# Kernel tuning notes

Hardware: AMD Instinct MI355X
Metric: run time of the kernel (lower is better)

Reference implementation:

```python
import jax, jax.numpy as jnp
import numpy as np

NUM_HEADS = 8
NEG_INF = -1e9  # stand-in for -inf in the causal mask (avoids nan under masked softmax)


def setup_inputs() -> dict:
    key = jax.random.key(0)
    ks = jax.random.split(key, 8)
    B, C, H, W = 2, 512, 64, 64
    E = 512
    s = 1.0 / np.sqrt(C)
    return {
        "query": jax.random.normal(ks[0], (B, C, H, W), jnp.float32),
        "key": jax.random.normal(ks[1], (B, C, H, W), jnp.float32),
        "Wq": jax.random.normal(ks[2], (E, C), jnp.float32) * s,
        "bq": jax.random.normal(ks[3], (E,), jnp.float32) * 0.01,
        "Wk": jax.random.normal(ks[4], (E, C), jnp.float32) * s,
        "bk": jax.random.normal(ks[5], (E,), jnp.float32) * 0.01,
        "Wv": jax.random.normal(ks[6], (E, C), jnp.float32) * s,
        "bv": jax.random.normal(ks[7], (E,), jnp.float32) * 0.01,
    }


def reference(query, key, Wq, bq, Wk, bk, Wv, bv):
    B, qdim, H, W = query.shape
    N = H * W
    E = Wq.shape[0]
    nh = NUM_HEADS
    hd = E // nh

    # (B, C, H, W) -> (B, N, C)
    q_tok = query.transpose(0, 2, 3, 1).reshape(B, N, qdim)
    k_tok = key.transpose(0, 2, 3, 1).reshape(B, N, key.shape[1])

    q = (q_tok @ Wq.T + bq).reshape(B, N, nh, hd)
    k = (k_tok @ Wk.T + bk).reshape(B, N, nh, hd)
    v = (k_tok @ Wv.T + bv).reshape(B, N, nh, hd)

    # scores: (B, heads, N, N)
    scores = jnp.einsum("bqhd,bkhd->bhqk", q, k) / jnp.sqrt(jnp.float32(hd))
    causal = jnp.tril(jnp.ones((N, N), dtype=bool))
    scores = jnp.where(causal, scores, NEG_INF)
    attn = jax.nn.softmax(scores, axis=-1)  # dropout p=0.0 -> identity

    x = jnp.einsum("bhqk,bkhd->bhqd", attn, v)  # (B, h, N, hd)
    # permute to (B, h, hd, N) then view as (B, E, H, W) — matches torch ordering
    out = x.transpose(0, 1, 3, 2).reshape(B, E, H, W)
    return out
```

## Files before the change

### kernel.cpp

```cpp
#include <hip/hip_runtime.h>


typedef __bf16 bf16;
typedef __attribute__((ext_vector_type(8))) __bf16 bf16x8;
typedef __attribute__((ext_vector_type(4))) float floatx4;

#define B_ 2
#define Cc 512
#define Nn 4096
#define Ee 512
#define NH 8
#define HD 64

#define QSCALE 0.1803368801111204f

__global__ __launch_bounds__(64) void detect_dtype(
    const unsigned short* __restrict__ w, int* __restrict__ flag) {
  bool bad = false;
#pragma unroll
  for (int i = 0; i < 16; ++i) {
    unsigned u = w[threadIdx.x * 16 + i];
    float v = __uint_as_float(u << 16);
    bad |= !(v > -1024.f && v < 1024.f);
  }
  unsigned long long b = __ballot(bad);
  if (threadIdx.x == 0) *flag = (b != 0ull) ? 1 : 0;
}

#define WSEG 262144
#define WTOT 787968

__device__ __forceinline__ bf16x8 load8e(const void* base, size_t eidx, int f32) {
  if (!f32) return *(const bf16x8*)((const bf16*)base + eidx);
  const float* f = (const float*)base + eidx;
  float4 a = *(const float4*)f;
  float4 c = *(const float4*)(f + 4);
  union { bf16 h[8]; bf16x8 v; } u;
  u.h[0] = (bf16)a.x; u.h[1] = (bf16)a.y; u.h[2] = (bf16)a.z; u.h[3] = (bf16)a.w;
  u.h[4] = (bf16)c.x; u.h[5] = (bf16)c.y; u.h[6] = (bf16)c.z; u.h[7] = (bf16)c.w;
  return u.v;
}

__global__ __launch_bounds__(256) void prep(
    const void* __restrict__ X0, const void* __restrict__ X1,
    bf16* __restrict__ T0, bf16* __restrict__ T1,
    const float* __restrict__ Wq, const float* __restrict__ Wk,
    const float* __restrict__ Wv, const float* __restrict__ bq,
    const float* __restrict__ bk, const float* __restrict__ bv,
    bf16* __restrict__ Wb, const int* __restrict__ flagp) {
  const int f32 = *flagp;
  if (blockIdx.z == 4) {
    if (!f32) return;
    int task = (int)blockIdx.y * 64 + (int)blockIdx.x;
    int idx = (task * 256 + (int)threadIdx.x) * 8;
    if (idx >= WTOT) return;
    const float* src;
    int off;
    if (idx < WSEG)            { src = Wq; off = idx; }
    else if (idx < 2 * WSEG)   { src = Wk; off = idx - WSEG; }
    else if (idx < 3 * WSEG)   { src = Wv; off = idx - 2 * WSEG; }
    else if (idx < 3 * WSEG + 512)  { src = bq; off = idx - 3 * WSEG; }
    else if (idx < 3 * WSEG + 1024) { src = bk; off = idx - 3 * WSEG - 512; }
    else                            { src = bv; off = idx - 3 * WSEG - 1024; }
    float4 a = *(const float4*)(src + off);
    float4 c = *(const float4*)(src + off + 4);
    union { bf16 h[8]; bf16x8 v; } u;
    u.h[0] = (bf16)a.x; u.h[1] = (bf16)a.y; u.h[2] = (bf16)a.z; u.h[3] = (bf16)a.w;
    u.h[4] = (bf16)c.x; u.h[5] = (bf16)c.y; u.h[6] = (bf16)c.z; u.h[7] = (bf16)c.w;
    *(bf16x8*)(Wb + idx) = u.v;
    return;
  }
  __shared__ __align__(16) bf16 T[64 * 64];
  const int z = blockIdx.z;
  const int bb = z & 1;
  const void* src = (z >> 1) ? X1 : X0;
  bf16* dst = (z >> 1) ? T1 : T0;
  const int n0 = blockIdx.x * 64, c0 = blockIdx.y * 64;
  const int t = threadIdx.x;
  const size_t sbase = ((size_t)bb * Cc + c0) * (size_t)Nn + n0;

#pragma unroll
  for (int it = 0; it < 2; ++it) {
    int task = t + it * 256;
    int crow = task >> 3, gr = task & 7;
    bf16x8 v = load8e(src, sbase + (size_t)crow * Nn + gr * 8, f32);
    int slot = gr ^ (crow & 7);
    *(bf16x8*)&T[crow * 64 + slot * 8] = v;
  }
  __syncthreads();
  const int nrow = t & 63, cp = t >> 6;
  bf16* db = dst + ((size_t)bb * Nn + n0 + nrow) * Cc + c0;
#pragma unroll
  for (int it = 0; it < 2; ++it) {
    int cg = cp * 2 + it;
    union { bf16 h[8]; bf16x8 v; } u;
#pragma unroll
    for (int j = 0; j < 8; ++j) {
      int c = cg * 8 + j;
      int slot = (nrow >> 3) ^ (c & 7);
      u.h[j] = T[c * 64 + slot * 8 + (nrow & 7)];
    }
    *(bf16x8*)(db + cg * 8) = u.v;
  }
}

__global__ __launch_bounds__(256) void gemm3(
    const bf16* __restrict__ Xtq, const bf16* __restrict__ Xtk,
    const void* __restrict__ Wq0, const bf16* __restrict__ Wqb,
    const void* __restrict__ Wk0, const bf16* __restrict__ Wkb,
    const void* __restrict__ Wv0, const bf16* __restrict__ Wvb,
    const void* __restrict__ bq0, const bf16* __restrict__ bqb,
    const void* __restrict__ bk0, const bf16* __restrict__ bkb,
    const void* __restrict__ bv0, const bf16* __restrict__ bvb,
    bf16* __restrict__ Qt, bf16* __restrict__ Kt, bf16* __restrict__ Vh,
    int zoff, const int* __restrict__ flagp) {
  const int f32 = *flagp;
  const int z = (int)blockIdx.z + zoff;
  const int op = z >> 1, b = z & 1;
  const bf16 *A, *Bt, *bias;
  bf16* Out;
  long sAb, sBb, sOb;
  int Nq, biasOnM, m0, n0;
  float scaleOut;
  if (op == 0) {
    A = Xtq; sAb = (long)Nn * Cc;
    Bt = f32 ? Wqb : (const bf16*)Wq0; sBb = 0;
    bias = f32 ? bqb : (const bf16*)bq0;
    Out = Qt; sOb = (long)Nn * Ee; Nq = Ee; biasOnM = 0; scaleOut = QSCALE;
    m0 = blockIdx.x * 128; n0 = blockIdx.y * 64;
  } else if (op == 1) {
    A = Xtk; sAb = (long)Nn * Cc;
    Bt = f32 ? Wkb : (const bf16*)Wk0; sBb = 0;
    bias = f32 ? bkb : (const bf16*)bk0;
    Out = Kt; sOb = (long)Nn * Ee; Nq = Ee; biasOnM = 0; scaleOut = 1.0f;
    m0 = blockIdx.x * 128; n0 = blockIdx.y * 64;
  } else {
    A = f32 ? Wvb : (const bf16*)Wv0; sAb = 0;
    Bt = Xtk; sBb = (long)Nn * Cc;
    bias = f32 ? bvb : (const bf16*)bv0;
    Out = Vh; sOb = (long)Ee * Nn; Nq = Nn; biasOnM = 1; scaleOut = 1.0f;
    m0 = (blockIdx.x >> 3) * 128;
    n0 = (blockIdx.y * 8 + (blockIdx.x & 7)) * 64;
  }
  constexpr int K = 512;
  constexpr int SA = 40;
  __shared__ __align__(16) bf16 As[2][128 * SA];
  __shared__ __align__(16) bf16 Bs[2][64 * SA];
  const int tid = threadIdx.x;
  const int lane = tid & 63, wave = tid >> 6;
  const int quad = lane >> 4, lm = lane & 15;
  const bf16* Ab = A + (size_t)b * sAb;
  const bf16* Bb = Bt + (size_t)b * sBb;
  bf16* Ob = Out + (size_t)b * sOb;

  const int arow = tid >> 2, ag = tid & 3;

  floatx4 acc[2][4];
#pragma unroll
  for (int i = 0; i < 2; ++i)
#pragma unroll
    for (int j = 0; j < 4; ++j) acc[i][j] = (floatx4){0.f, 0.f, 0.f, 0.f};

  bf16x8 pa0[2], pa1[2], pb0[2];
#define LOADG(s, step)                                                      \
  do {                                                                      \
    const int k0_ = (step) * 32;                                            \
    pa0[s] = *(const bf16x8*)(Ab + (size_t)(m0 + arow) * K + k0_ + ag * 8); \
    pa1[s] = *(const bf16x8*)(Ab + (size_t)(m0 + 64 + arow) * K + k0_ + ag * 8); \
    pb0[s] = *(const bf16x8*)(Bb + (size_t)(n0 + arow) * K + k0_ + ag * 8); \
  } while (0)
#define STAGEG(s, c_)                                                       \
  do {                                                                      \
    *(bf16x8*)&As[c_][arow * SA + ag * 8] = pa0[s];                         \
    *(bf16x8*)&As[c_][(64 + arow) * SA + ag * 8] = pa1[s];                  \
    *(bf16x8*)&Bs[c_][arow * SA + ag * 8] = pb0[s];                         \
  } while (0)

  LOADG(0, 0);
  LOADG(1, 1);
  STAGEG(0, 0);
  __syncthreads();

  for (int kk = 0; kk < 16; kk += 2) {
#pragma unroll
    for (int u = 0; u < 2; ++u) {
      const int t = kk + u;
      if (t + 2 < 16) LOADG(u, t + 2);
      bf16x8 af[2], bfr[4];
#pragma unroll
      for (int mf = 0; mf < 2; ++mf) {
        int r = wave * 32 + mf * 16 + lm;
        af[mf] = *(const bf16x8*)&As[u][r * SA + quad * 8];
      }
#pragma unroll
      for (int nf = 0; nf < 4; ++nf) {
        int r = nf * 16 + lm;
        bfr[nf] = *(const bf16x8*)&Bs[u][r * SA + quad * 8];
      }
      if (t + 1 < 16) STAGEG(u ^ 1, u ^ 1);
#pragma unroll
      for (int mf = 0; mf < 2; ++mf)
#pragma unroll
        for (int nf = 0; nf < 4; ++nf)
          acc[mf][nf] = __builtin_amdgcn_mfma_f32_16x16x32_bf16(
              af[mf], bfr[nf], acc[mf][nf], 0, 0, 0);
      __syncthreads();
    }
  }
#undef LOADG
#undef STAGEG

#pragma unroll
  for (int mf = 0; mf < 2; ++mf) {
#pragma unroll
    for (int nf = 0; nf < 4; ++nf) {
      int col = n0 + nf * 16 + lm;
      float bn = biasOnM ? 0.f : (float)bias[col];
#pragma unroll
      for (int r = 0; r < 4; ++r) {
        int rowg = m0 + wave * 32 + mf * 16 + quad * 4 + r;
        float bv = biasOnM ? (float)bias[rowg] : bn;
        Ob[(size_t)rowg * Nq + col] = (bf16)((acc[mf][nf][r] + bv) * scaleOut);
      }
    }
  }
}

__device__ __forceinline__ float fast_exp2(float x) {
  return __builtin_amdgcn_exp2f(x);
}
__device__ __forceinline__ unsigned pack_bf16_2(float a, float b) {
  unsigned ua = __float_as_uint(a) + 0x8000u;
  unsigned ub = __float_as_uint(b) + 0x8000u;
  return (ua >> 16) | (ub & 0xFFFF0000u);
}

__global__ __launch_bounds__(256, 4) void attn(
    const bf16* __restrict__ Qt, const bf16* __restrict__ Kt,
    const bf16* __restrict__ Ve, void* __restrict__ Out,
    const int* __restrict__ flagp) {
  const int f32 = *flagp;
  constexpr int SK = 72;
  __shared__ __align__(16) bf16 Ks[2][64 * SK];
  __shared__ __align__(16) bf16 Vs[2][64 * SK];
  const int tid = threadIdx.x, lane = tid & 63, w = tid >> 6;
  const int quad = lane >> 4, lm = lane & 15;

  const int L = (int)blockIdx.x + 64 * (int)blockIdx.y + 512 * (int)blockIdx.z;
  const int xcd = L & 7, slot0 = L >> 3;
  const int half = slot0 >> 6, sp = slot0 & 63;
  const int p = half ? 63 - sp : sp;
  const int hp = xcd * 2 + half;
  const int b = hp >> 3, h = hp & 7;

  const int Q0 = p * 64;
  const int qbase = Q0 + w * 16;
  const int last = p;

  bf16x8 qf[2];
  {
    const bf16* qp =
        Qt + ((size_t)b * Nn + qbase + lm) * Ee + h * HD + quad * 8;
    qf[0] = *(const bf16x8*)qp;
    qf[1] = *(const bf16x8*)(qp + 32);
  }
  floatx4 accO[4];
#pragma unroll
  for (int df = 0; df < 4; ++df) accO[df] = (floatx4){0.f, 0.f, 0.f, 0.f};
  float lsum = 0.f;

  const int r0 = tid >> 3, g = tid & 7;
  const int sslot = ((g + r0) & 7) * 8;
  const bf16* kp0 = Kt + ((size_t)b * Nn + r0) * Ee + h * HD + g * 8;
  const bf16* kp1 = kp0 + (size_t)32 * Ee;
  const bf16* vp0 = Ve + ((size_t)b * Ee + h * HD + r0) * Nn + g * 8;
  const bf16* vp1 = vp0 + (size_t)32 * Nn;

  const int rbase = ((lm >> 2) << 3) | (lm & 3);

  bf16x8 ka[2], kb[2], va[2], vb[2];
#define LOADT(s)                                                   \
  do {                                                             \
    ka[s] = *(const bf16x8*)kp0; kb[s] = *(const bf16x8*)kp1;      \
    va[s] = *(const bf16x8*)vp0; vb[s] = *(const bf16x8*)vp1;      \
    kp0 += (size_t)64 * Ee; kp1 += (size_t)64 * Ee;                \
    vp0 += 64; vp1 += 64;                                          \
  } while (0)
#define STAGET(s, buf)                                             \
  do {                                                             \
    *(bf16x8*)&Ks[buf][r0 * SK + sslot] = ka[s];                   \
    *(bf16x8*)&Ks[buf][(r0 + 32) * SK + sslot] = kb[s];            \
    *(bf16x8*)&Vs[buf][r0 * SK + sslot] = va[s];                   \
    *(bf16x8*)&Vs[buf][(r0 + 32) * SK + sslot] = vb[s];            \
  } while (0)

  LOADT(0);
  if (last >= 1) LOADT(1);
  STAGET(0, 0);
  __syncthreads();

#pragma unroll 1
  for (int kt = 0; kt <= last; kt += 2) {
#pragma unroll
    for (int u = 0; u < 2; ++u) {
      const int t = kt + u;
      if (u == 1 && t > last) break;
      const int k0 = t * 64;
      if (t + 2 <= last) LOADT(u);
      const bool skip = k0 > qbase + 15;

      bf16x8 pb[2];
      if (!skip) {
        floatx4 accS[4];
#pragma unroll
        for (int f = 0; f < 4; ++f) accS[f] = (floatx4){0.f, 0.f, 0.f, 0.f};
        __builtin_amdgcn_s_setprio(1);
#pragma unroll
        for (int ks = 0; ks < 2; ++ks)
#pragma unroll
          for (int f = 0; f < 4; ++f) {
            const int R = rbase + ((f & 1) << 2) + ((f >> 1) << 5);
            const int sl = (ks * 4 + quad + R) & 7;
            bf16x8 ak = *(const bf16x8*)&Ks[u][R * SK + sl * 8];
            accS[f] = __builtin_amdgcn_mfma_f32_16x16x32_bf16(
                ak, qf[ks], accS[f], 0, 0, 0);
          }
        __builtin_amdgcn_s_setprio(0);
        const bool maskt = (k0 + 63 > qbase);
        if (!maskt) {
          float la = 0.f, lb = 0.f;
#pragma unroll
          for (int g2 = 0; g2 < 2; ++g2) {
            union { unsigned pk[4]; bf16x8 v; } uu;
#pragma unroll
            for (int jp = 0; jp < 4; ++jp) {
              const int fidx = g2 * 2 + (jp >> 1);
              const int re = (jp & 1) * 2;
              float p0 = fast_exp2(accS[fidx][re]);
              float p1 = fast_exp2(accS[fidx][re + 1]);
              la += p0; lb += p1;
              uu.pk[jp] = pack_bf16_2(p0, p1);
            }
            pb[g2] = uu.v;
          }
          lsum += la + lb;
        } else {
          const int qg = qbase + lm;
          float la = 0.f, lb = 0.f;
#pragma unroll
          for (int g2 = 0; g2 < 2; ++g2) {
            union { unsigned pk[4]; bf16x8 v; } uu;
#pragma unroll
            for (int jp = 0; jp < 4; ++jp) {
              const int fidx = g2 * 2 + (jp >> 1);
              const int re = (jp & 1) * 2;
              const int key0 = k0 + g2 * 32 + quad * 8 + jp * 2;
              float p0 = fast_exp2(accS[fidx][re]);
              float p1 = fast_exp2(accS[fidx][re + 1]);
              if (key0 > qg) p0 = 0.f;
              if (key0 + 1 > qg) p1 = 0.f;
              la += p0; lb += p1;
              uu.pk[jp] = pack_bf16_2(p0, p1);
            }
            pb[g2] = uu.v;
          }
          lsum += la + lb;
        }
      }
      if (t + 1 <= last) STAGET(u ^ 1, u ^ 1);
      if (!skip) {
        __builtin_amdgcn_s_setprio(1);
#pragma unroll
        for (int g2 = 0; g2 < 2; ++g2)
#pragma unroll
          for (int df = 0; df < 4; ++df) {
            const int Rv = df * 16 + lm;
            const int sl = (g2 * 4 + quad + Rv) & 7;
            bf16x8 av = *(const bf16x8*)&Vs[u][Rv * SK + sl * 8];
            accO[df] = __builtin_amdgcn_mfma_f32_16x16x32_bf16(
                av, pb[g2], accO[df], 0, 0, 0);
          }
        __builtin_amdgcn_s_setprio(0);
      }
      __syncthreads();
    }
  }
#undef LOADT
#undef STAGET

  lsum += __shfl_xor(lsum, 16);
  lsum += __shfl_xor(lsum, 32);

  const float inv = 1.0f / lsum;
  const int qg = qbase + lm;
#pragma unroll
  for (int df = 0; df < 4; ++df) {
#pragma unroll
    for (int r = 0; r < 4; ++r) {
      int d = h * HD + df * 16 + quad * 4 + r;
      size_t off = ((size_t)b * Ee + d) * Nn + qg;
      if (!f32) ((bf16*)Out)[off] = (bf16)(accO[df][r] * inv);
      else      ((float*)Out)[off] = accO[df][r] * inv;
    }
  }
}

extern "C" void kernel_launch(void* const* d_in, const int* in_sizes, int n_in,
                              void* d_out, int out_size, void* d_ws,
                              size_t ws_size, hipStream_t stream) {
  const void* q  = d_in[0];
  const void* k  = d_in[1];
  const void* Wq = d_in[2];
  const void* bq = d_in[3];
  const void* Wk = d_in[4];
  const void* bk = d_in[5];
  const void* Wv = d_in[6];
  const void* bv = d_in[7];

  const size_t SZ = (size_t)B_ * Nn * Cc;
  int*  flag = (int*)d_ws;
  bf16* Xtq  = (bf16*)((char*)d_ws + 1024);
  bf16* Qt   = Xtq + SZ;
  bf16* Kt   = Qt + SZ;
  bf16* Xtk  = (bf16*)d_out;
  bf16* Wb   = (bf16*)((char*)d_out + 8 * 1024 * 1024);
  bf16* Wqb = Wb,            *Wkb = Wb + WSEG,    *Wvb = Wb + 2 * WSEG;
  bf16* bqb = Wb + 3 * WSEG, *bkb = bqb + 512,    *bvb = bqb + 1024;

  const size_t need = 1024 + 4 * SZ * sizeof(bf16);
  const bool sep = ws_size >= need;
  bf16* Vh = sep ? (Kt + SZ) : Xtq;

  detect_dtype<<<1, 64, 0, stream>>>((const unsigned short*)Wq, flag);
  prep<<<dim3(64, 8, 5), 256, 0, stream>>>(
      q, k, Xtq, Xtk,
      (const float*)Wq, (const float*)Wk, (const float*)Wv,
      (const float*)bq, (const float*)bk, (const float*)bv, Wb, flag);
  if (sep) {
    gemm3<<<dim3(32, 8, 6), 256, 0, stream>>>(
        Xtq, Xtk, Wq, Wqb, Wk, Wkb, Wv, Wvb,
        bq, bqb, bk, bkb, bv, bvb, Qt, Kt, Vh, 0, flag);
  } else {
    gemm3<<<dim3(32, 8, 4), 256, 0, stream>>>(
        Xtq, Xtk, Wq, Wqb, Wk, Wkb, Wv, Wvb,
        bq, bqb, bk, bkb, bv, bvb, Qt, Kt, Vh, 0, flag);
    gemm3<<<dim3(32, 8, 2), 256, 0, stream>>>(
        Xtq, Xtk, Wq, Wqb, Wk, Wkb, Wv, Wvb,
        bq, bqb, bk, bkb, bv, bvb, Qt, Kt, Vh, 4, flag);
  }
  attn<<<dim3(64, NH, B_), 256, 0, stream>>>(Qt, Kt, Vh, d_out, flag);
}
```

Baseline: 177.1 us.

## Drop dtype-detect kernel and widen GEMM tiles to 128x128

```diff
diff --git a/kernel.cpp b/kernel.cpp
--- a/kernel.cpp
+++ b/kernel.cpp
@@ -14,21 +14,19 @@
 
 #define QSCALE 0.1803368801111204f
 
-__global__ __launch_bounds__(64) void detect_dtype(
-    const unsigned short* __restrict__ w, int* __restrict__ flag) {
+#define WSEG 262144
+#define WTOT 787968
+
+__device__ __forceinline__ int probe_f32(const unsigned short* w, int tid) {
   bool bad = false;
 #pragma unroll
   for (int i = 0; i < 16; ++i) {
-    unsigned u = w[threadIdx.x * 16 + i];
+    unsigned u = w[(tid & 63) * 16 + i];
     float v = __uint_as_float(u << 16);
     bad |= !(v > -1024.f && v < 1024.f);
   }
-  unsigned long long b = __ballot(bad);
-  if (threadIdx.x == 0) *flag = (b != 0ull) ? 1 : 0;
-}
-
-#define WSEG 262144
-#define WTOT 787968
+  return (__ballot(bad) != 0ull) ? 1 : 0;
+}
 
 __device__ __forceinline__ bf16x8 load8e(const void* base, size_t eidx, int f32) {
   if (!f32) return *(const bf16x8*)((const bf16*)base + eidx);
@@ -47,8 +45,8 @@
     const float* __restrict__ Wq, const float* __restrict__ Wk,
     const float* __restrict__ Wv, const float* __restrict__ bq,
     const float* __restrict__ bk, const float* __restrict__ bv,
-    bf16* __restrict__ Wb, const int* __restrict__ flagp) {
-  const int f32 = *flagp;
+    bf16* __restrict__ Wb) {
+  const int f32 = probe_f32((const unsigned short*)Wq, (int)threadIdx.x);
   if (blockIdx.z == 4) {
     if (!f32) return;
     int task = (int)blockIdx.y * 64 + (int)blockIdx.x;
@@ -113,8 +111,8 @@
     const void* __restrict__ bk0, const bf16* __restrict__ bkb,
     const void* __restrict__ bv0, const bf16* __restrict__ bvb,
     bf16* __restrict__ Qt, bf16* __restrict__ Kt, bf16* __restrict__ Vh,
-    int zoff, const int* __restrict__ flagp) {
-  const int f32 = *flagp;
+    int zoff) {
+  const int f32 = probe_f32((const unsigned short*)Wq0, (int)threadIdx.x);
   const int z = (int)blockIdx.z + zoff;
   const int op = z >> 1, b = z & 1;
   const bf16 *A, *Bt, *bias;
@@ -127,25 +125,25 @@
     Bt = f32 ? Wqb : (const bf16*)Wq0; sBb = 0;
     bias = f32 ? bqb : (const bf16*)bq0;
     Out = Qt; sOb = (long)Nn * Ee; Nq = Ee; biasOnM = 0; scaleOut = QSCALE;
-    m0 = blockIdx.x * 128; n0 = blockIdx.y * 64;
+    m0 = blockIdx.x * 128; n0 = blockIdx.y * 128;
   } else if (op == 1) {
     A = Xtk; sAb = (long)Nn * Cc;
     Bt = f32 ? Wkb : (const bf16*)Wk0; sBb = 0;
     bias = f32 ? bkb : (const bf16*)bk0;
     Out = Kt; sOb = (long)Nn * Ee; Nq = Ee; biasOnM = 0; scaleOut = 1.0f;
-    m0 = blockIdx.x * 128; n0 = blockIdx.y * 64;
+    m0 = blockIdx.x * 128; n0 = blockIdx.y * 128;
   } else {
     A = f32 ? Wvb : (const bf16*)Wv0; sAb = 0;
     Bt = Xtk; sBb = (long)Nn * Cc;
     bias = f32 ? bvb : (const bf16*)bv0;
     Out = Vh; sOb = (long)Ee * Nn; Nq = Nn; biasOnM = 1; scaleOut = 1.0f;
-    m0 = (blockIdx.x >> 3) * 128;
-    n0 = (blockIdx.y * 8 + (blockIdx.x & 7)) * 64;
+    m0 = blockIdx.y * 128;
+    n0 = blockIdx.x * 128;
   }
   constexpr int K = 512;
   constexpr int SA = 40;
   __shared__ __align__(16) bf16 As[2][128 * SA];
-  __shared__ __align__(16) bf16 Bs[2][64 * SA];
+  __shared__ __align__(16) bf16 Bs[2][128 * SA];
   const int tid = threadIdx.x;
   const int lane = tid & 63, wave = tid >> 6;
   const int quad = lane >> 4, lm = lane & 15;
@@ -155,25 +153,27 @@
 
   const int arow = tid >> 2, ag = tid & 3;
 
-  floatx4 acc[2][4];
+  floatx4 acc[2][8];
 #pragma unroll
   for (int i = 0; i < 2; ++i)
 #pragma unroll
-    for (int j = 0; j < 4; ++j) acc[i][j] = (floatx4){0.f, 0.f, 0.f, 0.f};
-
-  bf16x8 pa0[2], pa1[2], pb0[2];
+    for (int j = 0; j < 8; ++j) acc[i][j] = (floatx4){0.f, 0.f, 0.f, 0.f};
+
+  bf16x8 pa0[2], pa1[2], pb0[2], pb1[2];
 #define LOADG(s, step)                                                      \
   do {                                                                      \
     const int k0_ = (step) * 32;                                            \
     pa0[s] = *(const bf16x8*)(Ab + (size_t)(m0 + arow) * K + k0_ + ag * 8); \
     pa1[s] = *(const bf16x8*)(Ab + (size_t)(m0 + 64 + arow) * K + k0_ + ag * 8); \
     pb0[s] = *(const bf16x8*)(Bb + (size_t)(n0 + arow) * K + k0_ + ag * 8); \
+    pb1[s] = *(const bf16x8*)(Bb + (size_t)(n0 + 64 + arow) * K + k0_ + ag * 8); \
   } while (0)
 #define STAGEG(s, c_)                                                       \
   do {                                                                      \
     *(bf16x8*)&As[c_][arow * SA + ag * 8] = pa0[s];                         \
     *(bf16x8*)&As[c_][(64 + arow) * SA + ag * 8] = pa1[s];                  \
     *(bf16x8*)&Bs[c_][arow * SA + ag * 8] = pb0[s];                         \
+    *(bf16x8*)&Bs[c_][(64 + arow) * SA + ag * 8] = pb1[s];                  \
   } while (0)
 
   LOADG(0, 0);
@@ -186,24 +186,22 @@
     for (int u = 0; u < 2; ++u) {
       const int t = kk + u;
       if (t + 2 < 16) LOADG(u, t + 2);
-      bf16x8 af[2], bfr[4];
+      bf16x8 af[2];
 #pragma unroll
       for (int mf = 0; mf < 2; ++mf) {
         int r = wave * 32 + mf * 16 + lm;
         af[mf] = *(const bf16x8*)&As[u][r * SA + quad * 8];
       }
-#pragma unroll
-      for (int nf = 0; nf < 4; ++nf) {
+      if (t + 1 < 16) STAGEG(u ^ 1, u ^ 1);
+#pragma unroll
+      for (int nf = 0; nf < 8; ++nf) {
         int r = nf * 16 + lm;
-        bfr[nf] = *(const bf16x8*)&Bs[u][r * SA + quad * 8];
+        bf16x8 bfr = *(const bf16x8*)&Bs[u][r * SA + quad * 8];
+        acc[0][nf] = __builtin_amdgcn_mfma_f32_16x16x32_bf16(
+            af[0], bfr, acc[0][nf], 0, 0, 0);
+        acc[1][nf] = __builtin_amdgcn_mfma_f32_16x16x32_bf16(
+            af[1], bfr, acc[1][nf], 0, 0, 0);
       }
-      if (t + 1 < 16) STAGEG(u ^ 1, u ^ 1);
-#pragma unroll
-      for (int mf = 0; mf < 2; ++mf)
-#pragma unroll
-        for (int nf = 0; nf < 4; ++nf)
-          acc[mf][nf] = __builtin_amdgcn_mfma_f32_16x16x32_bf16(
-              af[mf], bfr[nf], acc[mf][nf], 0, 0, 0);
       __syncthreads();
     }
   }
@@ -213,7 +211,7 @@
 #pragma unroll
   for (int mf = 0; mf < 2; ++mf) {
 #pragma unroll
-    for (int nf = 0; nf < 4; ++nf) {
+    for (int nf = 0; nf < 8; ++nf) {
       int col = n0 + nf * 16 + lm;
       float bn = biasOnM ? 0.f : (float)bias[col];
 #pragma unroll
@@ -238,12 +236,12 @@
 __global__ __launch_bounds__(256, 4) void attn(
     const bf16* __restrict__ Qt, const bf16* __restrict__ Kt,
     const bf16* __restrict__ Ve, void* __restrict__ Out,
-    const int* __restrict__ flagp) {
-  const int f32 = *flagp;
+    const unsigned short* __restrict__ wdet) {
+  const int tid = threadIdx.x, lane = tid & 63, w = tid >> 6;
+  const int f32 = probe_f32(wdet, tid);
   constexpr int SK = 72;
   __shared__ __align__(16) bf16 Ks[2][64 * SK];
   __shared__ __align__(16) bf16 Vs[2][64 * SK];
-  const int tid = threadIdx.x, lane = tid & 63, w = tid >> 6;
   const int quad = lane >> 4, lm = lane & 15;
 
   const int L = (int)blockIdx.x + 64 * (int)blockIdx.y + 512 * (int)blockIdx.z;
@@ -418,7 +416,6 @@
   const void* bv = d_in[7];
 
   const size_t SZ = (size_t)B_ * Nn * Cc;
-  int*  flag = (int*)d_ws;
   bf16* Xtq  = (bf16*)((char*)d_ws + 1024);
   bf16* Qt   = Xtq + SZ;
   bf16* Kt   = Qt + SZ;
@@ -431,22 +428,22 @@
   const bool sep = ws_size >= need;
   bf16* Vh = sep ? (Kt + SZ) : Xtq;
 
-  detect_dtype<<<1, 64, 0, stream>>>((const unsigned short*)Wq, flag);
   prep<<<dim3(64, 8, 5), 256, 0, stream>>>(
       q, k, Xtq, Xtk,
       (const float*)Wq, (const float*)Wk, (const float*)Wv,
-      (const float*)bq, (const float*)bk, (const float*)bv, Wb, flag);
+      (const float*)bq, (const float*)bk, (const float*)bv, Wb);
   if (sep) {
-    gemm3<<<dim3(32, 8, 6), 256, 0, stream>>>(
+    gemm3<<<dim3(32, 4, 6), 256, 0, stream>>>(
         Xtq, Xtk, Wq, Wqb, Wk, Wkb, Wv, Wvb,
-        bq, bqb, bk, bkb, bv, bvb, Qt, Kt, Vh, 0, flag);
+        bq, bqb, bk, bkb, bv, bvb, Qt, Kt, Vh, 0);
   } else {
-    gemm3<<<dim3(32, 8, 4), 256, 0, stream>>>(
+    gemm3<<<dim3(32, 4, 4), 256, 0, stream>>>(
         Xtq, Xtk, Wq, Wqb, Wk, Wkb, Wv, Wvb,
-        bq, bqb, bk, bkb, bv, bvb, Qt, Kt, Vh, 0, flag);
-    gemm3<<<dim3(32, 8, 2), 256, 0, stream>>>(
+        bq, bqb, bk, bkb, bv, bvb, Qt, Kt, Vh, 0);
+    gemm3<<<dim3(32, 4, 2), 256, 0, stream>>>(
         Xtq, Xtk, Wq, Wqb, Wk, Wkb, Wv, Wvb,
-        bq, bqb, bk, bkb, bv, bvb, Qt, Kt, Vh, 4, flag);
-  }
-  attn<<<dim3(64, NH, B_), 256, 0, stream>>>(Qt, Kt, Vh, d_out, flag);
-}
+        bq, bqb, bk, bkb, bv, bvb, Qt, Kt, Vh, 4);
+  }
+  attn<<<dim3(64, NH, B_), 256, 0, stream>>>(
+      Qt, Kt, Vh, d_out, (const unsigned short*)Wq);
+}
```

After: 175.9 us. About the same (-0.7%).
